# Kernel optimization log

Measured on AMD Instinct MI355X. Metric: run time of the kernel, lower is better.

Reference implementation:

```python
import jax, jax.numpy as jnp
import numpy as np

N = 50000      # nodes
E = 800000     # edges (avg degree 16)
D = 128        # in_dim = hidden_dim
C = 40         # num_classes
BN_EPS = 1e-5


def setup_inputs() -> dict:
    key = jax.random.key(0)
    ks = jax.random.split(key, 24)
    h = jax.random.normal(ks[0], (N, D), dtype=jnp.float32)
    edge_src = jax.random.randint(ks[1], (E,), 0, N)
    edge_dst = jax.random.randint(ks[2], (E,), 0, N)
    mask = jnp.ones((E, 1), dtype=jnp.float32)  # adj_mask2_fixed (frozen)

    def lin_w(k, fi, fo):
        return jax.random.normal(k, (fi, fo), dtype=jnp.float32) / np.sqrt(fi).astype(np.float32)

    def lin_b(k, fo):
        return jax.random.normal(k, (fo,), dtype=jnp.float32) * 0.01

    dims = [(D, D), (D, D), (D, C)]  # last GIN layer -> num_classes
    out = {"h": h, "edge_src": edge_src, "edge_dst": edge_dst, "mask": mask}
    for i, (fi, fo) in enumerate(dims):
        out[f"w{i}"] = lin_w(ks[3 + 4 * i], fi, fo)
        out[f"b{i}"] = lin_b(ks[4 + 4 * i], fo)
        out[f"g{i}"] = jnp.ones((fo,), jnp.float32) + 0.05 * jax.random.normal(ks[5 + 4 * i], (fo,), jnp.float32)
        out[f"beta{i}"] = 0.05 * jax.random.normal(ks[6 + 4 * i], (fo,), jnp.float32)
        out[f"rm{i}"] = 0.1 * jax.random.normal(jax.random.fold_in(key, 100 + i), (fo,), jnp.float32)
        out[f"rv{i}"] = jax.random.uniform(jax.random.fold_in(key, 200 + i), (fo,), jnp.float32, 0.5, 1.5)
    out["wp"] = lin_w(ks[20], D, C)
    out["bp"] = lin_b(ks[21], C)
    return out


def reference(h, edge_src, edge_dst, mask,
              w0, b0, g0, beta0, rm0, rv0,
              w1, b1, g1, beta1, rm1, rv1,
              w2, b2, g2, beta2, rm2, rv2,
              wp, bp):
    # in-degree for mean aggregation (DGL mean reducer: divide by in-degree,
    # zero for isolated nodes)
    ones_e = jnp.ones(edge_dst.shape, dtype=h.dtype)
    deg = jax.ops.segment_sum(ones_e, edge_dst, num_segments=N)
    deg_inv = jnp.where(deg > 0, 1.0 / jnp.maximum(deg, 1.0), 0.0)[:, None]

    def gin_layer(x, w, b, g, beta, rm, rv):
        msg = x[edge_src] * mask                                   # [E, d]
        agg = jax.ops.segment_sum(msg, edge_dst, num_segments=N) * deg_inv
        z = (x + agg) @ w + b                                      # (1+eps)=1, eps=0
        z = (z - rm) * jax.lax.rsqrt(rv + BN_EPS) * g + beta       # BN (eval, running stats)
        return jax.nn.relu(z)                                      # dropout: eval -> identity

    h1 = gin_layer(h, w0, b0, g0, beta0, rm0, rv0)    # [N, D]
    h2 = gin_layer(h1, w1, b1, g1, beta1, rm1, rv1)   # [N, D]  hidden_rep[-2]
    h3 = gin_layer(h2, w2, b2, g2, beta2, rm2, rv2)   # [N, C]  hidden_rep[-1]
    return ((h2 @ wp + bp) + h3) * 0.5
```

## Files before the change

### kernel.cpp

```cpp
#include <hip/hip_runtime.h>

#define N_NODES 50000
#define N_EDGES 800000
#define DIM 128
#define NCLS 40

#define NCHUNK 128
#define CE 6250
#define HALF_N 25088
#define WHALF 12544
#define SCAN_B 98
#define N_PAD 50432

typedef __bf16 bf16x8_t __attribute__((ext_vector_type(8)));
typedef unsigned short us8_t __attribute__((ext_vector_type(8)));
typedef float f32x4_t __attribute__((ext_vector_type(4)));

static __device__ __forceinline__ float b2f(unsigned short h) {
    unsigned u = ((unsigned)h) << 16;
    return __builtin_bit_cast(float, u);
}
static __device__ __forceinline__ unsigned short f2b(float f) {
    unsigned u = __builtin_bit_cast(unsigned, f);
    u += 0x7FFFu + ((u >> 16) & 1u);
    return (unsigned short)(u >> 16);
}

__global__ __launch_bounds__(256) void to_bf16(const float* __restrict__ in,
                                               unsigned short* __restrict__ out) {
    size_t e0 = ((size_t)blockIdx.x * 256 + threadIdx.x) * 8;
    f32x4_t v0 = *(const f32x4_t*)(in + e0);
    f32x4_t v1 = *(const f32x4_t*)(in + e0 + 4);
    us8_t o;
    #pragma unroll
    for (int j = 0; j < 4; ++j) { o[j] = f2b(v0[j]); o[4 + j] = f2b(v1[j]); }
    *(us8_t*)(out + e0) = o;
}

__global__ __launch_bounds__(256) void repack_w(const float* __restrict__ w0,
                                                const float* __restrict__ w1,
                                                const float* __restrict__ w2,
                                                const float* __restrict__ wp,
                                                unsigned short* __restrict__ f0h,
                                                unsigned short* __restrict__ f0l,
                                                unsigned short* __restrict__ f1h,
                                                unsigned short* __restrict__ f1l,
                                                unsigned short* __restrict__ f2h,
                                                unsigned short* __restrict__ f2l,
                                                unsigned short* __restrict__ fph,
                                                unsigned short* __restrict__ fpl) {
    int t = blockIdx.x * 256 + threadIdx.x;
    const float* src;
    unsigned short *dh, *dl;
    int idx, ncols;
    if (t < 16384)      { src = w0; dh = f0h; dl = f0l; idx = t;         ncols = 128; }
    else if (t < 32768) { src = w1; dh = f1h; dl = f1l; idx = t - 16384; ncols = 128; }
    else if (t < 38912) { src = w2; dh = f2h; dl = f2l; idx = t - 32768; ncols = 48; }
    else if (t < 45056) { src = wp; dh = fph; dl = fpl; idx = t - 38912; ncols = 48; }
    else return;
    int k = idx / ncols, n = idx - k * ncols;
    float v;
    if (ncols == 128) v = src[k * 128 + n];
    else              v = (n < NCLS) ? src[k * NCLS + n] : 0.f;
    int nt = n >> 4, m = n & 15, kt = k >> 5, quad = (k >> 3) & 3, j = k & 7;
    int off = ((nt * 4 + kt) * 64 + quad * 16 + m) * 8 + j;
    unsigned short hi = f2b(v);
    dh[off] = hi;
    dl[off] = f2b(v - b2f(hi));
}

__global__ __launch_bounds__(256) void chunk_count(const int* __restrict__ dst,
                                                   unsigned* __restrict__ cnt) {
    __shared__ unsigned lds[WHALF];
    int c = blockIdx.x, h = blockIdx.y, tid = threadIdx.x;
    for (int w = tid; w < WHALF; w += 256) lds[w] = 0;
    __syncthreads();
    int base = c * CE;
    for (int k = tid; k < CE; k += 256) {
        int local = dst[base + k] - h * HALF_N;
        if (local >= 0 && local < HALF_N)
            atomicAdd(&lds[local >> 1], 1u << ((local & 1) * 16));
    }
    __syncthreads();
    unsigned* out = cnt + ((size_t)(h * NCHUNK + c)) * WHALF;
    for (int w = tid; w < WHALF; w += 256) out[w] = lds[w];
}

__global__ __launch_bounds__(256) void cscan(unsigned* __restrict__ cnt,
                                             unsigned* __restrict__ degp,
                                             int* __restrict__ partial) {
    __shared__ int lds[256];
    int b = blockIdx.x;
    int h = b / 49;
    int w = (b % 49) * 256 + threadIdx.x;
    unsigned acc = 0;
    for (int c = 0; c < NCHUNK; ++c) {
        size_t idx = ((size_t)(h * NCHUNK + c)) * WHALF + w;
        unsigned v = cnt[idx];
        cnt[idx] = acc;
        acc += v;
    }
    degp[h * WHALF + w] = acc;
    lds[threadIdx.x] = (int)(acc & 0xFFFFu) + (int)(acc >> 16);
    __syncthreads();
    #pragma unroll
    for (int off = 128; off > 0; off >>= 1) {
        if (threadIdx.x < off) lds[threadIdx.x] += lds[threadIdx.x + off];
        __syncthreads();
    }
    if (threadIdx.x == 0) partial[b] = lds[0];
}

__global__ __launch_bounds__(128) void scan_blocks(const int* __restrict__ partial,
                                                   int* __restrict__ blk_off) {
    __shared__ int lds[128];
    int tid = threadIdx.x;
    lds[tid] = (tid < SCAN_B) ? partial[tid] : 0;
    __syncthreads();
    #pragma unroll
    for (int off = 1; off < 128; off <<= 1) {
        int v = lds[tid];
        int add = (tid >= off) ? lds[tid - off] : 0;
        __syncthreads();
        lds[tid] = v + add;
        __syncthreads();
    }
    if (tid < SCAN_B) blk_off[tid] = (tid == 0) ? 0 : lds[tid - 1];
}

__global__ __launch_bounds__(256) void scan_final(const unsigned* __restrict__ degp,
                                                  const int* __restrict__ blk_off,
                                                  int* __restrict__ rs,
                                                  int* __restrict__ deg,
                                                  float* __restrict__ dinv) {
    __shared__ int lds[256];
    int b = blockIdx.x;
    int h = b / 49;
    int tid = threadIdx.x;
    int w = (b % 49) * 256 + tid;
    unsigned dp = degp[h * WHALF + w];
    int lo = (int)(dp & 0xFFFFu), hi = (int)(dp >> 16);
    int s = lo + hi;
    lds[tid] = s;
    __syncthreads();
    #pragma unroll
    for (int off = 1; off < 256; off <<= 1) {
        int v = lds[tid];
        int add = (tid >= off) ? lds[tid - off] : 0;
        __syncthreads();
        lds[tid] = v + add;
        __syncthreads();
    }
    int excl = blk_off[b] + lds[tid] - s;
    int n0 = h * HALF_N + 2 * w;
    rs[n0] = excl;
    rs[n0 + 1] = excl + lo;
    deg[n0] = lo;
    deg[n0 + 1] = hi;
    dinv[n0] = (lo > 0) ? (1.0f / (float)lo) : 0.0f;
    dinv[n0 + 1] = (hi > 0) ? (1.0f / (float)hi) : 0.0f;
}

__global__ __launch_bounds__(256) void fill2(const int* __restrict__ src,
                                             const int* __restrict__ dst,
                                             const float* __restrict__ mask,
                                             const unsigned* __restrict__ cnt,
                                             const int* __restrict__ rs,
                                             unsigned* __restrict__ csr) {
    __shared__ unsigned cur[WHALF];
    int c = blockIdx.x, h = blockIdx.y, tid = threadIdx.x;
    const unsigned* off = cnt + ((size_t)(h * NCHUNK + c)) * WHALF;
    for (int w = tid; w < WHALF; w += 256) cur[w] = off[w];
    __syncthreads();
    int base = c * CE;
    for (int k = tid; k < CE; k += 256) {
        int e = base + k;
        int d = dst[e];
        int local = d - h * HALF_N;
        if (local >= 0 && local < HALF_N) {
            unsigned sm = (unsigned)src[e] | ((unsigned)f2b(mask[e]) << 16);
            int sh = (local & 1) * 16;
            unsigned old = atomicAdd(&cur[local >> 1], 1u << sh);
            int rank = (int)((old >> sh) & 0xFFFFu);
            csr[rs[d] + rank] = sm;
        }
    }
}

static __device__ __forceinline__ void gather4(const unsigned short* __restrict__ xb,
                                               const float* __restrict__ xres,
                                               const int* __restrict__ rs,
                                               const int* __restrict__ deg,
                                               const float* __restrict__ dinv,
                                               const unsigned* __restrict__ csr,
                                               int nb0, int lane,
                                               float (*ldsrow)[132], int row0) {
    int rs4[4], dg4[4];
    float di4[4];
    #pragma unroll
    for (int i = 0; i < 4; ++i) {
        int n = nb0 + i;
        rs4[i] = rs[n];
        dg4[i] = deg[n];
        di4[i] = dinv[n];
    }
    int nb_pre = dg4[0] < 16 ? dg4[0] : 16;
    unsigned pk_pre = (lane < nb_pre) ? csr[rs4[0] + lane] : 0;
    #pragma unroll
    for (int i = 0; i < 4; ++i) {
        int cnt = dg4[i], start = rs4[i];
        unsigned pk = pk_pre;
        if (i < 3) {
            int nbn = dg4[i + 1] < 16 ? dg4[i + 1] : 16;
            pk_pre = (lane < nbn) ? csr[rs4[i + 1] + lane] : 0;
        }
        float acc0 = 0.f, acc1 = 0.f;
        for (int base = 0; base < cnt; base += 16) {
            if (base > 0) {
                int nb = cnt - base;
                if (nb > 16) nb = 16;
                pk = (lane < nb) ? csr[start + base + lane] : 0;
            }
            unsigned vv[16];
            float mm[16];
            #pragma unroll
            for (int j = 0; j < 16; ++j) {
                unsigned p = (unsigned)__builtin_amdgcn_readlane((int)pk, j);
                mm[j] = b2f((unsigned short)(p >> 16));
                vv[j] = *(const unsigned*)(xb + (size_t)(p & 0xFFFFu) * DIM + lane * 2);
            }
            #pragma unroll
            for (int j = 0; j < 16; ++j) {
                acc0 += mm[j] * b2f((unsigned short)(vv[j] & 0xFFFFu));
                acc1 += mm[j] * b2f((unsigned short)(vv[j] >> 16));
            }
        }
        float di = di4[i];
        float2 xp = *(const float2*)(xres + (size_t)(nb0 + i) * DIM + lane * 2);
        ldsrow[row0 + i][lane * 2]     = xp.x + acc0 * di;
        ldsrow[row0 + i][lane * 2 + 1] = xp.y + acc1 * di;
    }
}

__global__ __launch_bounds__(256) void fused_layer(const unsigned short* __restrict__ xb,
                                                   const float* __restrict__ x,
                                                   const int* __restrict__ rs,
                                                   const int* __restrict__ deg,
                                                   const float* __restrict__ dinv,
                                                   const unsigned* __restrict__ csr,
                                                   const unsigned short* __restrict__ wfh,
                                                   const unsigned short* __restrict__ wfl,
                                                   const float* __restrict__ bias,
                                                   const float* __restrict__ gam,
                                                   const float* __restrict__ bet,
                                                   const float* __restrict__ rm,
                                                   const float* __restrict__ rv,
                                                   float* __restrict__ out,
                                                   unsigned short* __restrict__ outb) {
    __shared__ float lds[16][132];
    int tid = threadIdx.x;
    int wave = tid >> 6, lane = tid & 63;
    int rbase = blockIdx.x * 16;

    gather4(xb, x, rs, deg, dinv, csr, rbase + wave * 4, lane, lds, wave * 4);
    __syncthreads();

    int m = lane & 15, quad = lane >> 4;
    const float* ap = &lds[m][0];

    us8_t ah[4], al[4];
    #pragma unroll
    for (int kt = 0; kt < 4; ++kt) {
        f32x4_t p0 = *(const f32x4_t*)(ap + kt * 32 + quad * 8);
        f32x4_t p1 = *(const f32x4_t*)(ap + kt * 32 + quad * 8 + 4);
        #pragma unroll
        for (int j = 0; j < 4; ++j) {
            unsigned short h0 = f2b(p0[j]);
            unsigned short h1 = f2b(p1[j]);
            ah[kt][j] = h0;
            ah[kt][4 + j] = h1;
            al[kt][j] = f2b(p0[j] - b2f(h0));
            al[kt][4 + j] = f2b(p1[j] - b2f(h1));
        }
    }

    f32x4_t acc[2] = {};
    #pragma unroll
    for (int kt = 0; kt < 4; ++kt) {
        #pragma unroll
        for (int t = 0; t < 2; ++t) {
            int nt = wave * 2 + t;
            int boff = ((nt * 4 + kt) * 64 + lane) * 8;
            us8_t bh = *(const us8_t*)(wfh + boff);
            us8_t bl = *(const us8_t*)(wfl + boff);
            acc[t] = __builtin_amdgcn_mfma_f32_16x16x32_bf16(
                __builtin_bit_cast(bf16x8_t, ah[kt]),
                __builtin_bit_cast(bf16x8_t, bh), acc[t], 0, 0, 0);
            acc[t] = __builtin_amdgcn_mfma_f32_16x16x32_bf16(
                __builtin_bit_cast(bf16x8_t, ah[kt]),
                __builtin_bit_cast(bf16x8_t, bl), acc[t], 0, 0, 0);
            acc[t] = __builtin_amdgcn_mfma_f32_16x16x32_bf16(
                __builtin_bit_cast(bf16x8_t, al[kt]),
                __builtin_bit_cast(bf16x8_t, bh), acc[t], 0, 0, 0);
        }
    }

    #pragma unroll
    for (int t = 0; t < 2; ++t) {
        int nt = wave * 2 + t;
        int j = nt * 16 + m;
        float bj = bias[j];
        float sc = gam[j] * rsqrtf(rv[j] + 1e-5f);
        float sh = bet[j] - rm[j] * sc;
        #pragma unroll
        for (int i = 0; i < 4; ++i) {
            int r = rbase + quad * 4 + i;
            float z = fmaxf((acc[t][i] + bj) * sc + sh, 0.f);
            out[(size_t)r * DIM + j] = z;
            outb[(size_t)r * DIM + j] = f2b(z);
        }
    }
}

__global__ __launch_bounds__(256) void fused_final2(const unsigned short* __restrict__ xb,
                                                    const float* __restrict__ h2,
                                                    const int* __restrict__ rs,
                                                    const int* __restrict__ deg,
                                                    const float* __restrict__ dinv,
                                                    const unsigned* __restrict__ csr,
                                                    const unsigned short* __restrict__ f2h,
                                                    const unsigned short* __restrict__ f2l,
                                                    const unsigned short* __restrict__ fph,
                                                    const unsigned short* __restrict__ fpl,
                                                    const float* __restrict__ b2,
                                                    const float* __restrict__ g2,
                                                    const float* __restrict__ be2,
                                                    const float* __restrict__ rm2,
                                                    const float* __restrict__ rv2,
                                                    const float* __restrict__ bp,
                                                    float* __restrict__ out) {
    __shared__ float lds[16][132];
    int tid = threadIdx.x;
    int wave = tid >> 6, lane = tid & 63;
    int rbase = blockIdx.x * 16;

    gather4(xb, h2, rs, deg, dinv, csr, rbase + wave * 4, lane, lds, wave * 4);
    __syncthreads();

    if (wave == 3) return;

    int m = lane & 15, quad = lane >> 4;
    int arow = rbase + m;
    const float* ap2 = &lds[m][0];
    const float* aph = h2 + (size_t)arow * DIM;

    us8_t a2h[4], a2l[4], ahh[4], ahl[4];
    #pragma unroll
    for (int kt = 0; kt < 4; ++kt) {
        f32x4_t p0 = *(const f32x4_t*)(ap2 + kt * 32 + quad * 8);
        f32x4_t p1 = *(const f32x4_t*)(ap2 + kt * 32 + quad * 8 + 4);
        f32x4_t q0 = *(const f32x4_t*)(aph + kt * 32 + quad * 8);
        f32x4_t q1 = *(const f32x4_t*)(aph + kt * 32 + quad * 8 + 4);
        #pragma unroll
        for (int j = 0; j < 4; ++j) {
            unsigned short h0 = f2b(p0[j]), h1 = f2b(p1[j]);
            a2h[kt][j] = h0; a2h[kt][4 + j] = h1;
            a2l[kt][j] = f2b(p0[j] - b2f(h0));
            a2l[kt][4 + j] = f2b(p1[j] - b2f(h1));
            unsigned short g0 = f2b(q0[j]), g1 = f2b(q1[j]);
            ahh[kt][j] = g0; ahh[kt][4 + j] = g1;
            ahl[kt][j] = f2b(q0[j] - b2f(g0));
            ahl[kt][4 + j] = f2b(q1[j] - b2f(g1));
        }
    }

    int nt = wave;
    f32x4_t acc2 = {};
    f32x4_t accp = {};
    #pragma unroll
    for (int kt = 0; kt < 4; ++kt) {
        int boff = ((nt * 4 + kt) * 64 + lane) * 8;
        us8_t b2hv = *(const us8_t*)(f2h + boff);
        us8_t b2lv = *(const us8_t*)(f2l + boff);
        us8_t bphv = *(const us8_t*)(fph + boff);
        us8_t bplv = *(const us8_t*)(fpl + boff);
        acc2 = __builtin_amdgcn_mfma_f32_16x16x32_bf16(
            __builtin_bit_cast(bf16x8_t, a2h[kt]),
            __builtin_bit_cast(bf16x8_t, b2hv), acc2, 0, 0, 0);
        acc2 = __builtin_amdgcn_mfma_f32_16x16x32_bf16(
            __builtin_bit_cast(bf16x8_t, a2h[kt]),
            __builtin_bit_cast(bf16x8_t, b2lv), acc2, 0, 0, 0);
        acc2 = __builtin_amdgcn_mfma_f32_16x16x32_bf16(
            __builtin_bit_cast(bf16x8_t, a2l[kt]),
            __builtin_bit_cast(bf16x8_t, b2hv), acc2, 0, 0, 0);
        accp = __builtin_amdgcn_mfma_f32_16x16x32_bf16(
            __builtin_bit_cast(bf16x8_t, ahh[kt]),
            __builtin_bit_cast(bf16x8_t, bphv), accp, 0, 0, 0);
        accp = __builtin_amdgcn_mfma_f32_16x16x32_bf16(
            __builtin_bit_cast(bf16x8_t, ahh[kt]),
            __builtin_bit_cast(bf16x8_t, bplv), accp, 0, 0, 0);
        accp = __builtin_amdgcn_mfma_f32_16x16x32_bf16(
            __builtin_bit_cast(bf16x8_t, ahl[kt]),
            __builtin_bit_cast(bf16x8_t, bphv), accp, 0, 0, 0);
    }

    int j = nt * 16 + m;
    if (j < NCLS) {
        float b2j = b2[j];
        float sc = g2[j] * rsqrtf(rv2[j] + 1e-5f);
        float sh = be2[j] - rm2[j] * sc;
        float bpj = bp[j];
        #pragma unroll
        for (int i = 0; i < 4; ++i) {
            int r = rbase + quad * 4 + i;
            float z = fmaxf((acc2[i] + b2j) * sc + sh, 0.f);
            float p = accp[i] + bpj;
            out[(size_t)r * NCLS + j] = (p + z) * 0.5f;
        }
    }
}

extern "C" void kernel_launch(void* const* d_in, const int* in_sizes, int n_in,
                              void* d_out, int out_size, void* d_ws, size_t ws_size,
                              hipStream_t stream) {
    const float* h    = (const float*)d_in[0];
    const int* esrc   = (const int*)d_in[1];
    const int* edst   = (const int*)d_in[2];
    const float* mask = (const float*)d_in[3];
    const float* w0   = (const float*)d_in[4];
    const float* b0   = (const float*)d_in[5];
    const float* g0   = (const float*)d_in[6];
    const float* be0  = (const float*)d_in[7];
    const float* rm0  = (const float*)d_in[8];
    const float* rv0  = (const float*)d_in[9];
    const float* w1   = (const float*)d_in[10];
    const float* b1   = (const float*)d_in[11];
    const float* g1   = (const float*)d_in[12];
    const float* be1  = (const float*)d_in[13];
    const float* rm1  = (const float*)d_in[14];
    const float* rv1  = (const float*)d_in[15];
    const float* w2   = (const float*)d_in[16];
    const float* b2   = (const float*)d_in[17];
    const float* g2   = (const float*)d_in[18];
    const float* be2  = (const float*)d_in[19];
    const float* rm2  = (const float*)d_in[20];
    const float* rv2  = (const float*)d_in[21];
    const float* wp   = (const float*)d_in[22];
    const float* bp   = (const float*)d_in[23];

    char* ws = (char*)d_ws;
    size_t off = 0;
    auto alloc = [&](size_t bytes) {
        char* p = ws + off;
        off = (off + bytes + 255) & ~(size_t)255;
        return p;
    };
    int* rs       = (int*)alloc(N_PAD * 4);
    int* deg      = (int*)alloc(N_PAD * 4);
    float* dinv   = (float*)alloc(N_PAD * 4);
    int* partial  = (int*)alloc(128 * 4);
    int* blk_off  = (int*)alloc(128 * 4);
    unsigned* degp = (unsigned*)alloc(2 * WHALF * 4);
    unsigned* csr = (unsigned*)alloc((size_t)N_EDGES * 4);
    unsigned* cnt = (unsigned*)alloc((size_t)2 * NCHUNK * WHALF * 4);
    float* hbA    = (float*)alloc((size_t)N_NODES * DIM * 4);
    float* hbB    = (float*)alloc((size_t)N_NODES * DIM * 4);
    unsigned short* xb16  = (unsigned short*)alloc((size_t)N_NODES * DIM * 2);
    unsigned short* hbA16 = (unsigned short*)alloc((size_t)N_NODES * DIM * 2);
    unsigned short* hbB16 = (unsigned short*)alloc((size_t)N_NODES * DIM * 2);
    unsigned short* f0h = (unsigned short*)alloc(16384 * 2);
    unsigned short* f0l = (unsigned short*)alloc(16384 * 2);
    unsigned short* f1h = (unsigned short*)alloc(16384 * 2);
    unsigned short* f1l = (unsigned short*)alloc(16384 * 2);
    unsigned short* f2h = (unsigned short*)alloc(6144 * 2);
    unsigned short* f2l = (unsigned short*)alloc(6144 * 2);
    unsigned short* fph = (unsigned short*)alloc(6144 * 2);
    unsigned short* fpl = (unsigned short*)alloc(6144 * 2);

    const int GB16 = N_NODES / 16;

    to_bf16<<<3125, 256, 0, stream>>>(h, xb16);
    repack_w<<<176, 256, 0, stream>>>(w0, w1, w2, wp, f0h, f0l, f1h, f1l,
                                      f2h, f2l, fph, fpl);
    chunk_count<<<dim3(NCHUNK, 2), 256, 0, stream>>>(edst, cnt);
    cscan<<<SCAN_B, 256, 0, stream>>>(cnt, degp, partial);
    scan_blocks<<<1, 128, 0, stream>>>(partial, blk_off);
    scan_final<<<SCAN_B, 256, 0, stream>>>(degp, blk_off, rs, deg, dinv);
    fill2<<<dim3(NCHUNK, 2), 256, 0, stream>>>(esrc, edst, mask, cnt, rs, csr);

    fused_layer<<<GB16, 256, 0, stream>>>(xb16, h, rs, deg, dinv, csr,
                                          f0h, f0l, b0, g0, be0, rm0, rv0, hbA, hbA16);
    fused_layer<<<GB16, 256, 0, stream>>>(hbA16, hbA, rs, deg, dinv, csr,
                                          f1h, f1l, b1, g1, be1, rm1, rv1, hbB, hbB16);
    fused_final2<<<GB16, 256, 0, stream>>>(hbB16, hbB, rs, deg, dinv, csr,
                                           f2h, f2l, fph, fpl,
                                           b2, g2, be2, rm2, rv2, bp, (float*)d_out);
}
```

Before: 310.8 us.

## Merge prep kernels, fold block scan into scan_final, double-buffer neighbor gathers

Merges the bf16 conversion and the weight repack into one launch. scan_blocks is removed: each scan_final block now reduces the partial sums of earlier blocks itself. The gather loop is software-pipelined, so CSR index loads and the 16-row feature gathers for the next node are issued before accumulating the current node, using two register buffers. This hides gather latency and cuts launch overhead, at the cost of higher register pressure and some redundant per-block reduction work.

```diff
diff --git a/kernel.cpp b/kernel.cpp
--- a/kernel.cpp
+++ b/kernel.cpp
@@ -26,30 +26,31 @@
     return (unsigned short)(u >> 16);
 }
 
-__global__ __launch_bounds__(256) void to_bf16(const float* __restrict__ in,
-                                               unsigned short* __restrict__ out) {
-    size_t e0 = ((size_t)blockIdx.x * 256 + threadIdx.x) * 8;
-    f32x4_t v0 = *(const f32x4_t*)(in + e0);
-    f32x4_t v1 = *(const f32x4_t*)(in + e0 + 4);
-    us8_t o;
-    #pragma unroll
-    for (int j = 0; j < 4; ++j) { o[j] = f2b(v0[j]); o[4 + j] = f2b(v1[j]); }
-    *(us8_t*)(out + e0) = o;
-}
-
-__global__ __launch_bounds__(256) void repack_w(const float* __restrict__ w0,
-                                                const float* __restrict__ w1,
-                                                const float* __restrict__ w2,
-                                                const float* __restrict__ wp,
-                                                unsigned short* __restrict__ f0h,
-                                                unsigned short* __restrict__ f0l,
-                                                unsigned short* __restrict__ f1h,
-                                                unsigned short* __restrict__ f1l,
-                                                unsigned short* __restrict__ f2h,
-                                                unsigned short* __restrict__ f2l,
-                                                unsigned short* __restrict__ fph,
-                                                unsigned short* __restrict__ fpl) {
-    int t = blockIdx.x * 256 + threadIdx.x;
+__global__ __launch_bounds__(256) void prep(const float* __restrict__ hsrc,
+                                            unsigned short* __restrict__ hout,
+                                            const float* __restrict__ w0,
+                                            const float* __restrict__ w1,
+                                            const float* __restrict__ w2,
+                                            const float* __restrict__ wp,
+                                            unsigned short* __restrict__ f0h,
+                                            unsigned short* __restrict__ f0l,
+                                            unsigned short* __restrict__ f1h,
+                                            unsigned short* __restrict__ f1l,
+                                            unsigned short* __restrict__ f2h,
+                                            unsigned short* __restrict__ f2l,
+                                            unsigned short* __restrict__ fph,
+                                            unsigned short* __restrict__ fpl) {
+    if (blockIdx.x < 3125) {
+        size_t e0 = ((size_t)blockIdx.x * 256 + threadIdx.x) * 8;
+        f32x4_t v0 = *(const f32x4_t*)(hsrc + e0);
+        f32x4_t v1 = *(const f32x4_t*)(hsrc + e0 + 4);
+        us8_t o;
+        #pragma unroll
+        for (int j = 0; j < 4; ++j) { o[j] = f2b(v0[j]); o[4 + j] = f2b(v1[j]); }
+        *(us8_t*)(hout + e0) = o;
+        return;
+    }
+    int t = (blockIdx.x - 3125) * 256 + threadIdx.x;
     const float* src;
     unsigned short *dh, *dl;
     int idx, ncols;
@@ -111,25 +112,8 @@
     if (threadIdx.x == 0) partial[b] = lds[0];
 }
 
-__global__ __launch_bounds__(128) void scan_blocks(const int* __restrict__ partial,
-                                                   int* __restrict__ blk_off) {
-    __shared__ int lds[128];
-    int tid = threadIdx.x;
-    lds[tid] = (tid < SCAN_B) ? partial[tid] : 0;
-    __syncthreads();
-    #pragma unroll
-    for (int off = 1; off < 128; off <<= 1) {
-        int v = lds[tid];
-        int add = (tid >= off) ? lds[tid - off] : 0;
-        __syncthreads();
-        lds[tid] = v + add;
-        __syncthreads();
-    }
-    if (tid < SCAN_B) blk_off[tid] = (tid == 0) ? 0 : lds[tid - 1];
-}
-
 __global__ __launch_bounds__(256) void scan_final(const unsigned* __restrict__ degp,
-                                                  const int* __restrict__ blk_off,
+                                                  const int* __restrict__ partial,
                                                   int* __restrict__ rs,
                                                   int* __restrict__ deg,
                                                   float* __restrict__ dinv) {
@@ -138,6 +122,15 @@
     int h = b / 49;
     int tid = threadIdx.x;
     int w = (b % 49) * 256 + tid;
+    lds[tid] = (tid < b) ? partial[tid] : 0;
+    __syncthreads();
+    #pragma unroll
+    for (int off = 128; off > 0; off >>= 1) {
+        if (tid < off) lds[tid] += lds[tid + off];
+        __syncthreads();
+    }
+    int boff = lds[0];
+    __syncthreads();
     unsigned dp = degp[h * WHALF + w];
     int lo = (int)(dp & 0xFFFFu), hi = (int)(dp >> 16);
     int s = lo + hi;
@@ -151,7 +144,7 @@
         lds[tid] = v + add;
         __syncthreads();
     }
-    int excl = blk_off[b] + lds[tid] - s;
+    int excl = boff + lds[tid] - s;
     int n0 = h * HALF_N + 2 * w;
     rs[n0] = excl;
     rs[n0 + 1] = excl + lo;
@@ -187,6 +180,25 @@
     }
 }
 
+static __device__ __forceinline__ void issue16(const unsigned short* __restrict__ xb,
+                                               unsigned pk, int lane, unsigned* vv) {
+    #pragma unroll
+    for (int j = 0; j < 16; ++j) {
+        unsigned p = (unsigned)__builtin_amdgcn_readlane((int)pk, j);
+        vv[j] = *(const unsigned*)(xb + (size_t)(p & 0xFFFFu) * DIM + lane * 2);
+    }
+}
+static __device__ __forceinline__ void accum16(unsigned pk, const unsigned* vv,
+                                               float& acc0, float& acc1) {
+    #pragma unroll
+    for (int j = 0; j < 16; ++j) {
+        unsigned p = (unsigned)__builtin_amdgcn_readlane((int)pk, j);
+        float mm = b2f((unsigned short)(p >> 16));
+        acc0 += mm * b2f((unsigned short)(vv[j] & 0xFFFFu));
+        acc1 += mm * b2f((unsigned short)(vv[j] >> 16));
+    }
+}
+
 static __device__ __forceinline__ void gather4(const unsigned short* __restrict__ xb,
                                                const float* __restrict__ xres,
                                                const int* __restrict__ rs,
@@ -204,36 +216,30 @@
         dg4[i] = deg[n];
         di4[i] = dinv[n];
     }
-    int nb_pre = dg4[0] < 16 ? dg4[0] : 16;
-    unsigned pk_pre = (lane < nb_pre) ? csr[rs4[0] + lane] : 0;
+    unsigned pk0, pk1, pk2, pk3;
+    pk0 = (lane < (dg4[0] < 16 ? dg4[0] : 16)) ? csr[rs4[0] + lane] : 0u;
+    pk1 = (lane < (dg4[1] < 16 ? dg4[1] : 16)) ? csr[rs4[1] + lane] : 0u;
+
+    unsigned vvA[16], vvB[16];
+    issue16(xb, pk0, lane, vvA);
+
+    unsigned pkq[4] = {pk0, pk1, 0u, 0u};
     #pragma unroll
     for (int i = 0; i < 4; ++i) {
-        int cnt = dg4[i], start = rs4[i];
-        unsigned pk = pk_pre;
-        if (i < 3) {
-            int nbn = dg4[i + 1] < 16 ? dg4[i + 1] : 16;
-            pk_pre = (lane < nbn) ? csr[rs4[i + 1] + lane] : 0;
-        }
+        if (i == 0) pk2 = (lane < (dg4[2] < 16 ? dg4[2] : 16)) ? csr[rs4[2] + lane] : 0u;
+        if (i == 1) pk3 = (lane < (dg4[3] < 16 ? dg4[3] : 16)) ? csr[rs4[3] + lane] : 0u;
+        if (i == 0) pkq[2] = pk2;
+        if (i == 1) pkq[3] = pk3;
+        if (i < 3) issue16(xb, pkq[i + 1], lane, (i & 1) ? vvA : vvB);
         float acc0 = 0.f, acc1 = 0.f;
-        for (int base = 0; base < cnt; base += 16) {
-            if (base > 0) {
-                int nb = cnt - base;
-                if (nb > 16) nb = 16;
-                pk = (lane < nb) ? csr[start + base + lane] : 0;
-            }
-            unsigned vv[16];
-            float mm[16];
-            #pragma unroll
-            for (int j = 0; j < 16; ++j) {
-                unsigned p = (unsigned)__builtin_amdgcn_readlane((int)pk, j);
-                mm[j] = b2f((unsigned short)(p >> 16));
-                vv[j] = *(const unsigned*)(xb + (size_t)(p & 0xFFFFu) * DIM + lane * 2);
-            }
-            #pragma unroll
-            for (int j = 0; j < 16; ++j) {
-                acc0 += mm[j] * b2f((unsigned short)(vv[j] & 0xFFFFu));
-                acc1 += mm[j] * b2f((unsigned short)(vv[j] >> 16));
-            }
+        accum16(pkq[i], (i & 1) ? vvB : vvA, acc0, acc1);
+        for (int base = 16; base < dg4[i]; base += 16) {
+            int nb = dg4[i] - base;
+            if (nb > 16) nb = 16;
+            unsigned pke = (lane < nb) ? csr[rs4[i] + base + lane] : 0u;
+            unsigned vvE[16];
+            issue16(xb, pke, lane, vvE);
+            accum16(pke, vvE, acc0, acc1);
         }
         float di = di4[i];
         float2 xp = *(const float2*)(xres + (size_t)(nb0 + i) * DIM + lane * 2);
@@ -459,7 +465,6 @@
     int* deg      = (int*)alloc(N_PAD * 4);
     float* dinv   = (float*)alloc(N_PAD * 4);
     int* partial  = (int*)alloc(128 * 4);
-    int* blk_off  = (int*)alloc(128 * 4);
     unsigned* degp = (unsigned*)alloc(2 * WHALF * 4);
     unsigned* csr = (unsigned*)alloc((size_t)N_EDGES * 4);
     unsigned* cnt = (unsigned*)alloc((size_t)2 * NCHUNK * WHALF * 4);
@@ -479,13 +484,11 @@
 
     const int GB16 = N_NODES / 16;
 
-    to_bf16<<<3125, 256, 0, stream>>>(h, xb16);
-    repack_w<<<176, 256, 0, stream>>>(w0, w1, w2, wp, f0h, f0l, f1h, f1l,
-                                      f2h, f2l, fph, fpl);
+    prep<<<3301, 256, 0, stream>>>(h, xb16, w0, w1, w2, wp,
+                                   f0h, f0l, f1h, f1l, f2h, f2l, fph, fpl);
     chunk_count<<<dim3(NCHUNK, 2), 256, 0, stream>>>(edst, cnt);
     cscan<<<SCAN_B, 256, 0, stream>>>(cnt, degp, partial);
-    scan_blocks<<<1, 128, 0, stream>>>(partial, blk_off);
-    scan_final<<<SCAN_B, 256, 0, stream>>>(degp, blk_off, rs, deg, dinv);
+    scan_final<<<SCAN_B, 256, 0, stream>>>(degp, partial, rs, deg, dinv);
     fill2<<<dim3(NCHUNK, 2), 256, 0, stream>>>(esrc, edst, mask, cnt, rs, csr);
 
     fused_layer<<<GB16, 256, 0, stream>>>(xb16, h, rs, deg, dinv, csr,
```

Result: faster. 299.9 us (-3.5%).
